# Kernel optimization log

Measured on AMD Instinct MI355X. Metric: run time of the kernel, lower is better.

The kernel has to match this reference:

```python
import jax, jax.numpy as jnp
import numpy as np

D_MODEL = 64
D_K = 64
D_V = 64
SEQ = 8192
MASK_VAL = 10.0 ** 10  # matches original: scores - 1e10 * triu_mask


def setup_inputs() -> dict:
    key = jax.random.key(0)
    ks = jax.random.split(key, 7)
    s = 1.0 / np.sqrt(D_MODEL)
    return {
        "x": jax.random.normal(ks[0], (SEQ, D_MODEL), dtype=jnp.float32),
        "w_q": jax.random.uniform(ks[1], (D_K, D_MODEL), jnp.float32, -s, s),
        "b_q": jax.random.uniform(ks[2], (D_K,), jnp.float32, -s, s),
        "w_k": jax.random.uniform(ks[3], (D_K, D_MODEL), jnp.float32, -s, s),
        "b_k": jax.random.uniform(ks[4], (D_K,), jnp.float32, -s, s),
        "w_v": jax.random.uniform(ks[5], (D_V, D_MODEL), jnp.float32, -s, s),
        "b_v": jax.random.uniform(ks[6], (D_V,), jnp.float32, -s, s),
    }


def reference(x, w_q, b_q, w_k, b_k, w_v, b_v):
    # torch Linear: y = x @ W.T + b
    q = x @ w_q.T + b_q            # [S, d_k]
    k = x @ w_k.T + b_k            # [S, d_k]
    v = x @ w_v.T + b_v            # [S, d_v]
    scores = (q @ k.T) / jnp.sqrt(jnp.float32(D_K))  # [S, S]
    S = scores.shape[0]
    # upper-triangular (strict) causal mask, subtracted with large constant
    mask = jnp.triu(jnp.ones((S, S), dtype=scores.dtype), k=1)
    attn = jax.nn.softmax(scores - MASK_VAL * mask, axis=1)
    return attn @ v                # [S, d_v]
```

## Files before the change

### kernel.cpp

```cpp
#include <hip/hip_runtime.h>

#define SEQ 8192
#define DM 64

typedef __bf16 bfrag __attribute__((ext_vector_type(8)));
typedef __bf16 b4v   __attribute__((ext_vector_type(4)));
typedef float  f4    __attribute__((ext_vector_type(4)));

union PW { int w[4]; bfrag v; };

#define QSCALE 0.1803368801111204f

__device__ inline float fexp2(float x) {
    float y;
    asm("v_exp_f32 %0, %1" : "=v"(y) : "v"(x));
    return y;
}

__device__ inline int cvtpk(float a, float b) {
    int d;
    asm("v_cvt_pk_bf16_f32 %0, %1, %2" : "=v"(d) : "v"(a), "v"(b));
    return d;
}

__device__ inline void split8(const float* __restrict__ p, bfrag& hi, bfrag& lo) {
    #pragma unroll
    for (int e = 0; e < 8; ++e) {
        const float v = p[e];
        const __bf16 h = (__bf16)v;
        hi[e] = h;
        lo[e] = (__bf16)(v - (float)h);
    }
}

__global__ __launch_bounds__(256) void qkv_proj(
    const float* __restrict__ x,
    const float* __restrict__ wq, const float* __restrict__ bq,
    const float* __restrict__ wk, const float* __restrict__ bk,
    const float* __restrict__ wv, const float* __restrict__ bv,
    __bf16* __restrict__ Qb, __bf16* __restrict__ Ks, __bf16* __restrict__ Vg)
{
    const int lane = threadIdx.x & 63;
    const int wid  = threadIdx.x >> 6;
    const int task = blockIdx.x * 4 + wid;
    const int rt   = task >> 2;
    const int dt   = task & 3;
    const int rb   = rt << 4;
    const int g = lane >> 4, r = lane & 15;

    bfrag xhi[2], xlo[2];
    #pragma unroll
    for (int kh = 0; kh < 2; ++kh)
        split8(x + (rb + r) * DM + kh * 32 + g * 8, xhi[kh], xlo[kh]);

    #pragma unroll
    for (int m = 0; m < 2; ++m) {
        const float* w    = m ? wk : wq;
        const float* bias = m ? bk : bq;
        bfrag whi[2], wlo[2];
        #pragma unroll
        for (int kh = 0; kh < 2; ++kh)
            split8(w + (dt * 16 + r) * DM + kh * 32 + g * 8, whi[kh], wlo[kh]);
        f4 acc = {0.f, 0.f, 0.f, 0.f};
        #pragma unroll
        for (int kh = 0; kh < 2; ++kh) {
            acc = __builtin_amdgcn_mfma_f32_16x16x32_bf16(whi[kh], xhi[kh], acc, 0, 0, 0);
            acc = __builtin_amdgcn_mfma_f32_16x16x32_bf16(wlo[kh], xhi[kh], acc, 0, 0, 0);
            acc = __builtin_amdgcn_mfma_f32_16x16x32_bf16(whi[kh], xlo[kh], acc, 0, 0, 0);
        }
        const int c0 = dt * 16 + g * 4;
        const float4 b4 = *(const float4*)(bias + c0);
        const float sc = (m == 0) ? QSCALE : 1.0f;
        b4v pv;
        pv[0] = (__bf16)((acc[0] + b4.x) * sc);
        pv[1] = (__bf16)((acc[1] + b4.y) * sc);
        pv[2] = (__bf16)((acc[2] + b4.z) * sc);
        pv[3] = (__bf16)((acc[3] + b4.w) * sc);
        if (m == 0) {
            *(b4v*)(Qb + (rb + r) * DM + c0) = pv;
        } else {
            const int row = rb + r, t = row >> 5, row32 = row & 31;
            const int ch  = dt * 2 + (g >> 1);
            const int b2  = ((row32 >> 4) << 1) | (ch >> 2);
            *(b4v*)(Ks + t * 2048 + b2 * 512 + (ch & 3) * 128
                       + (row32 & 15) * 8 + (g & 1) * 4) = pv;
        }
    }

    {
        bfrag whi[2], wlo[2];
        #pragma unroll
        for (int kh = 0; kh < 2; ++kh)
            split8(wv + (dt * 16 + r) * DM + kh * 32 + g * 8, whi[kh], wlo[kh]);
        f4 acc = {0.f, 0.f, 0.f, 0.f};
        #pragma unroll
        for (int kh = 0; kh < 2; ++kh) {
            acc = __builtin_amdgcn_mfma_f32_16x16x32_bf16(xhi[kh], whi[kh], acc, 0, 0, 0);
            acc = __builtin_amdgcn_mfma_f32_16x16x32_bf16(xlo[kh], whi[kh], acc, 0, 0, 0);
            acc = __builtin_amdgcn_mfma_f32_16x16x32_bf16(xhi[kh], wlo[kh], acc, 0, 0, 0);
        }
        const int d  = dt * 16 + r;
        const float bd = bv[d];
        const int L0 = (rb & 31) + g * 4;
        const int P0 = ((L0 & 15) >> 2) * 8 + (L0 >> 4) * 4;
        const int t  = rb >> 5;
        b4v pv;
        pv[0] = (__bf16)(acc[0] + bd);
        pv[1] = (__bf16)(acc[1] + bd);
        pv[2] = (__bf16)(acc[2] + bd);
        pv[3] = (__bf16)(acc[3] + bd);
        *(b4v*)(Vg + t * 2048 + (d >> 4) * 512 + (P0 >> 3) * 128
                   + (d & 15) * 8 + (P0 & 7)) = pv;
    }
}

__global__ __launch_bounds__(256)
__attribute__((amdgpu_waves_per_eu(4)))
void flash_attn(
    const __bf16* __restrict__ Qb, const __bf16* __restrict__ Ks,
    const __bf16* __restrict__ Vg,
    float* __restrict__ Opart, float* __restrict__ Lpart)
{
    __shared__ __align__(16) unsigned char smem[34816];

    const int tid  = threadIdx.x;
    const int lane = tid & 63;
    const int wid  = tid >> 6;
    const int b    = blockIdx.x;
    const int fam  = b >> 2;
    const int g4   = b & 3;
    const int grp  = fam >> 6, hh = fam & 63;
    const int qt   = (grp == 0) ? (255 - hh) : (grp == 1) ? hh
                   : (grp == 2) ? (191 - hh) : (64 + hh);
    const int qbase = qt * 32;
    const int gq = lane >> 4;
    const int r  = lane & 15;
    const int lo16 = lane << 4;

    bfrag qf[2][2];
    #pragma unroll
    for (int sub = 0; sub < 2; ++sub)
        #pragma unroll
        for (int kh = 0; kh < 2; ++kh)
            qf[sub][kh] = *(const bfrag*)(Qb + (qbase + sub * 16 + r) * DM + kh * 32 + gq * 8);

    bfrag ones;
    #pragma unroll
    for (int e = 0; e < 8; ++e) ones[e] = (__bf16)1.0f;

    f4 o[2][4] = {};
    f4 lsacc[2] = {};

    const char* Kbb = (const char*)Ks;
    const char* Vbb = (const char*)Vg;

    const int jw = g4 * 4 + wid;
    const int nlive = (qt >= jw) ? ((qt - jw) >> 4) + 1 : 0;

    for (int s = 0; s < nlive; ++s) {
        const int j = jw + s * 16;
        const long long jb = (long long)j * 4096;
        const bfrag kf0 = *(const bfrag*)(Kbb + jb + lo16);
        const bfrag kf1 = *(const bfrag*)(Kbb + jb + 1024 + lo16);
        const bfrag kf2 = *(const bfrag*)(Kbb + jb + 2048 + lo16);
        const bfrag kf3 = *(const bfrag*)(Kbb + jb + 3072 + lo16);
        bfrag vf[4];
        #pragma unroll
        for (int dt = 0; dt < 4; ++dt)
            vf[dt] = *(const bfrag*)(Vbb + jb + dt * 1024 + lo16);

        const int kvb = j * 32 + gq * 4;
        #pragma unroll
        for (int sub = 0; sub < 2; ++sub) {
            f4 sh0 = {}, sh1 = {};
            sh0 = __builtin_amdgcn_mfma_f32_16x16x32_bf16(kf0, qf[sub][0], sh0, 0, 0, 0);
            sh0 = __builtin_amdgcn_mfma_f32_16x16x32_bf16(kf1, qf[sub][1], sh0, 0, 0, 0);
            sh1 = __builtin_amdgcn_mfma_f32_16x16x32_bf16(kf2, qf[sub][0], sh1, 0, 0, 0);
            sh1 = __builtin_amdgcn_mfma_f32_16x16x32_bf16(kf3, qf[sub][1], sh1, 0, 0, 0);

            float p0[4], p1[4];
            if (j < qt) {
                #pragma unroll
                for (int e = 0; e < 4; ++e) {
                    p0[e] = fexp2(sh0[e]);
                    p1[e] = fexp2(sh1[e]);
                }
            } else {
                const int qg = qbase + sub * 16 + r;
                #pragma unroll
                for (int e = 0; e < 4; ++e) {
                    p0[e] = (kvb + e      <= qg) ? fexp2(sh0[e]) : 0.f;
                    p1[e] = (kvb + e + 16 <= qg) ? fexp2(sh1[e]) : 0.f;
                }
            }

            PW pu;
            pu.w[0] = cvtpk(p0[0], p0[1]); pu.w[1] = cvtpk(p0[2], p0[3]);
            pu.w[2] = cvtpk(p1[0], p1[1]); pu.w[3] = cvtpk(p1[2], p1[3]);

            lsacc[sub] = __builtin_amdgcn_mfma_f32_16x16x32_bf16(pu.v, ones, lsacc[sub], 0, 0, 0);
            #pragma unroll
            for (int dt = 0; dt < 4; ++dt)
                o[sub][dt] = __builtin_amdgcn_mfma_f32_16x16x32_bf16(pu.v, vf[dt], o[sub][dt], 0, 0, 0);
        }
    }

    float* Ol  = (float*)smem;
    float* Lsm = (float*)(smem + 33792);
    #pragma unroll
    for (int sub = 0; sub < 2; ++sub) {
        if (r == 0)
            #pragma unroll
            for (int e = 0; e < 4; ++e)
                Lsm[wid * 32 + sub * 16 + gq * 4 + e] = lsacc[sub][e];
        #pragma unroll
        for (int dt = 0; dt < 4; ++dt)
            #pragma unroll
            for (int e = 0; e < 4; ++e)
                Ol[(wid * 32 + sub * 16 + gq * 4 + e) * 66 + dt * 16 + r] = o[sub][dt][e];
    }
    __syncthreads();

    for (int i = tid; i < 32 * 64; i += 256) {
        const int row = i >> 6, col = i & 63;
        const float sum = Ol[(row) * 66 + col] + Ol[(32 + row) * 66 + col]
                        + Ol[(64 + row) * 66 + col] + Ol[(96 + row) * 66 + col];
        Opart[((long long)g4 * SEQ + qbase + row) * DM + col] = sum;
    }
    if (tid < 32) {
        const float l = Lsm[tid] + Lsm[32 + tid] + Lsm[64 + tid] + Lsm[96 + tid];
        Lpart[g4 * SEQ + qbase + tid] = l;
    }
}

__global__ __launch_bounds__(256) void normalize(
    const float* __restrict__ Opart, const float* __restrict__ Lpart,
    float* __restrict__ out)
{
    const int i = blockIdx.x * 256 + threadIdx.x;
    const f4* O = (const f4*)Opart;
    const int N = SEQ * DM / 4;
    const int row = i >> 4;
    const f4 a0 = O[i], a1 = O[N + i], a2 = O[2 * N + i], a3 = O[3 * N + i];
    const float l = (Lpart[row] + Lpart[SEQ + row])
                  + (Lpart[2 * SEQ + row] + Lpart[3 * SEQ + row]);
    const float inv = 1.0f / l;
    f4 res;
    #pragma unroll
    for (int e = 0; e < 4; ++e) res[e] = ((a0[e] + a1[e]) + (a2[e] + a3[e])) * inv;
    ((f4*)out)[i] = res;
}

extern "C" void kernel_launch(void* const* d_in, const int* in_sizes, int n_in,
                              void* d_out, int out_size, void* d_ws, size_t ws_size,
                              hipStream_t stream)
{
    (void)in_sizes; (void)n_in; (void)out_size; (void)ws_size;
    const float* x  = (const float*)d_in[0];
    const float* wq = (const float*)d_in[1];
    const float* bq = (const float*)d_in[2];
    const float* wk = (const float*)d_in[3];
    const float* bk = (const float*)d_in[4];
    const float* wv = (const float*)d_in[5];
    const float* bv = (const float*)d_in[6];
    float* out = (float*)d_out;

    __bf16* Qb = (__bf16*)d_ws;
    __bf16* Ks = Qb + SEQ * DM;
    __bf16* Vg = Ks + SEQ * DM;
    float*  Opart = (float*)(Vg + SEQ * DM);
    float*  Lpart = Opart + 4 * SEQ * DM;

    qkv_proj<<<512, 256, 0, stream>>>(x, wq, bq, wk, bk, wv, bv, Qb, Ks, Vg);
    flash_attn<<<1024, 256, 0, stream>>>(Qb, Ks, Vg, Opart, Lpart);
    normalize<<<SEQ * DM / 4 / 256, 256, 0, stream>>>(Opart, Lpart, out);
}
```

Baseline: 32.50 us.

## Use 8-wave blocks for flash attention and halve key-split partials

```diff
diff --git a/kernel.cpp b/kernel.cpp
--- a/kernel.cpp
+++ b/kernel.cpp
@@ -114,21 +114,22 @@
     }
 }
 
-__global__ __launch_bounds__(256)
+__global__ __launch_bounds__(512)
 __attribute__((amdgpu_waves_per_eu(4)))
 void flash_attn(
     const __bf16* __restrict__ Qb, const __bf16* __restrict__ Ks,
     const __bf16* __restrict__ Vg,
     float* __restrict__ Opart, float* __restrict__ Lpart)
 {
-    __shared__ __align__(16) unsigned char smem[34816];
+    __shared__ float Ol[4][32][66];
+    __shared__ float Lsm[8][32];
 
     const int tid  = threadIdx.x;
     const int lane = tid & 63;
     const int wid  = tid >> 6;
     const int b    = blockIdx.x;
-    const int fam  = b >> 2;
-    const int g4   = b & 3;
+    const int fam  = b >> 1;
+    const int slice = b & 1;
     const int grp  = fam >> 6, hh = fam & 63;
     const int qt   = (grp == 0) ? (255 - hh) : (grp == 1) ? hh
                    : (grp == 2) ? (191 - hh) : (64 + hh);
@@ -154,7 +155,7 @@
     const char* Kbb = (const char*)Ks;
     const char* Vbb = (const char*)Vg;
 
-    const int jw = g4 * 4 + wid;
+    const int jw = slice * 8 + wid;
     const int nlive = (qt >= jw) ? ((qt - jw) >> 4) + 1 : 0;
 
     for (int s = 0; s < nlive; ++s) {
@@ -205,31 +206,44 @@
         }
     }
 
-    float* Ol  = (float*)smem;
-    float* Lsm = (float*)(smem + 33792);
-    #pragma unroll
-    for (int sub = 0; sub < 2; ++sub) {
-        if (r == 0)
+    if (r == 0)
+        #pragma unroll
+        for (int sub = 0; sub < 2; ++sub)
             #pragma unroll
             for (int e = 0; e < 4; ++e)
-                Lsm[wid * 32 + sub * 16 + gq * 4 + e] = lsacc[sub][e];
-        #pragma unroll
-        for (int dt = 0; dt < 4; ++dt)
-            #pragma unroll
-            for (int e = 0; e < 4; ++e)
-                Ol[(wid * 32 + sub * 16 + gq * 4 + e) * 66 + dt * 16 + r] = o[sub][dt][e];
+                Lsm[wid][sub * 16 + gq * 4 + e] = lsacc[sub][e];
+
+    if (wid < 4) {
+        #pragma unroll
+        for (int sub = 0; sub < 2; ++sub)
+            #pragma unroll
+            for (int dt = 0; dt < 4; ++dt)
+                #pragma unroll
+                for (int e = 0; e < 4; ++e)
+                    Ol[wid][sub * 16 + gq * 4 + e][dt * 16 + r] = o[sub][dt][e];
     }
     __syncthreads();
-
-    for (int i = tid; i < 32 * 64; i += 256) {
+    if (wid >= 4) {
+        #pragma unroll
+        for (int sub = 0; sub < 2; ++sub)
+            #pragma unroll
+            for (int dt = 0; dt < 4; ++dt)
+                #pragma unroll
+                for (int e = 0; e < 4; ++e)
+                    Ol[wid - 4][sub * 16 + gq * 4 + e][dt * 16 + r] += o[sub][dt][e];
+    }
+    __syncthreads();
+
+    for (int i = tid; i < 32 * 64; i += 512) {
         const int row = i >> 6, col = i & 63;
-        const float sum = Ol[(row) * 66 + col] + Ol[(32 + row) * 66 + col]
-                        + Ol[(64 + row) * 66 + col] + Ol[(96 + row) * 66 + col];
-        Opart[((long long)g4 * SEQ + qbase + row) * DM + col] = sum;
+        const float sum = (Ol[0][row][col] + Ol[1][row][col])
+                        + (Ol[2][row][col] + Ol[3][row][col]);
+        Opart[((long long)slice * SEQ + qbase + row) * DM + col] = sum;
     }
     if (tid < 32) {
-        const float l = Lsm[tid] + Lsm[32 + tid] + Lsm[64 + tid] + Lsm[96 + tid];
-        Lpart[g4 * SEQ + qbase + tid] = l;
+        const float l = ((Lsm[0][tid] + Lsm[1][tid]) + (Lsm[2][tid] + Lsm[3][tid]))
+                      + ((Lsm[4][tid] + Lsm[5][tid]) + (Lsm[6][tid] + Lsm[7][tid]));
+        Lpart[slice * SEQ + qbase + tid] = l;
     }
 }
 
@@ -241,13 +255,11 @@
     const f4* O = (const f4*)Opart;
     const int N = SEQ * DM / 4;
     const int row = i >> 4;
-    const f4 a0 = O[i], a1 = O[N + i], a2 = O[2 * N + i], a3 = O[3 * N + i];
-    const float l = (Lpart[row] + Lpart[SEQ + row])
-                  + (Lpart[2 * SEQ + row] + Lpart[3 * SEQ + row]);
-    const float inv = 1.0f / l;
+    const f4 a0 = O[i], a1 = O[N + i];
+    const float inv = 1.0f / (Lpart[row] + Lpart[SEQ + row]);
     f4 res;
     #pragma unroll
-    for (int e = 0; e < 4; ++e) res[e] = ((a0[e] + a1[e]) + (a2[e] + a3[e])) * inv;
+    for (int e = 0; e < 4; ++e) res[e] = (a0[e] + a1[e]) * inv;
     ((f4*)out)[i] = res;
 }
 
@@ -269,9 +281,9 @@
     __bf16* Ks = Qb + SEQ * DM;
     __bf16* Vg = Ks + SEQ * DM;
     float*  Opart = (float*)(Vg + SEQ * DM);
-    float*  Lpart = Opart + 4 * SEQ * DM;
+    float*  Lpart = Opart + 2 * SEQ * DM;
 
     qkv_proj<<<512, 256, 0, stream>>>(x, wq, bq, wk, bk, wv, bv, Qb, Ks, Vg);
-    flash_attn<<<1024, 256, 0, stream>>>(Qb, Ks, Vg, Opart, Lpart);
+    flash_attn<<<512, 512, 0, stream>>>(Qb, Ks, Vg, Opart, Lpart);
     normalize<<<SEQ * DM / 4 / 256, 256, 0, stream>>>(Opart, Lpart, out);
 }
```

Measured after the change: 34.55 us. +6.3%, slower.
